# Kernel optimization log

Hardware: AMD Instinct MI355X
Metric: run time of the kernel (lower is better)

## Reference

```python
import jax, jax.numpy as jnp
import numpy as np

N_NODES = 50000
N_EDGES = 1600000
IN_FEATS = 128
HIDDEN = 128
NUM_CLASSES = 40


def setup_inputs() -> dict:
    key = jax.random.key(0)
    k1, k2, k3, k4, k5 = jax.random.split(key, 5)
    features = jax.random.normal(k1, (N_NODES, IN_FEATS), dtype=jnp.float32)
    src = jax.random.randint(k2, (N_EDGES,), 0, N_NODES, dtype=jnp.int32)
    dst = jax.random.randint(k3, (N_EDGES,), 0, N_NODES, dtype=jnp.int32)
    W1 = jax.random.normal(k4, (IN_FEATS, HIDDEN), dtype=jnp.float32) / np.sqrt(IN_FEATS)
    b1 = jnp.zeros((HIDDEN,), dtype=jnp.float32)
    W2 = jax.random.normal(k5, (HIDDEN, NUM_CLASSES), dtype=jnp.float32) / np.sqrt(HIDDEN)
    b2 = jnp.zeros((NUM_CLASSES,), dtype=jnp.float32)
    return {"features": features, "src": src, "dst": dst,
            "W1": W1, "b1": b1, "W2": W2, "b2": b2}


def _degree_norms(src, dst, n_nodes):
    ones = jnp.ones(src.shape[0], dtype=jnp.float32)
    deg_out = jax.ops.segment_sum(ones, src, num_segments=n_nodes)
    deg_in = jax.ops.segment_sum(ones, dst, num_segments=n_nodes)
    # DGL GraphConv clamps degree at 1 (zero-degree nodes get norm 1)
    norm_src = jax.lax.rsqrt(jnp.maximum(deg_out, 1.0))
    norm_dst = jax.lax.rsqrt(jnp.maximum(deg_in, 1.0))
    return norm_src, norm_dst


def _graph_conv(x, W, b, src, dst, norm_src, norm_dst, n_nodes):
    # norm='both': h = D_in^{-1/2} A^T (D_out^{-1/2} x W) + b
    h = (x * norm_src[:, None]) @ W          # [N, out]
    msgs = h[src]                             # gather  [E, out]
    agg = jax.ops.segment_sum(msgs, dst, num_segments=n_nodes)  # scatter-add [N, out]
    return agg * norm_dst[:, None] + b


def reference(features, src, dst, W1, b1, W2, b2):
    n = features.shape[0]
    norm_src, norm_dst = _degree_norms(src, dst, n)
    h = jax.nn.relu(_graph_conv(features, W1, b1, src, dst, norm_src, norm_dst, n))
    h = _graph_conv(h, W2, b2, src, dst, norm_src, norm_dst, n)
    return h
```

## Files before the change

### kernel.cpp

```cpp
#include <hip/hip_runtime.h>


#define CHUNK 16384
#define CHUNK_SHIFT 14
#define NSLICES 64

typedef int iv4 __attribute__((ext_vector_type(4)));
typedef short short8 __attribute__((ext_vector_type(8)));
typedef float f32x4 __attribute__((ext_vector_type(4)));

__device__ __forceinline__ unsigned f2bf_bits(float f) {
    unsigned u = __float_as_uint(f);
    return (u + 0x7FFFu + ((u >> 16) & 1u)) >> 16;
}
__device__ __forceinline__ unsigned pack_bf2(float a, float b) {
    return f2bf_bits(a) | (f2bf_bits(b) << 16);
}
__device__ __forceinline__ float bflo(unsigned v) { return __uint_as_float(v << 16); }
__device__ __forceinline__ float bfhi(unsigned v) { return __uint_as_float(v & 0xFFFF0000u); }


__global__ __launch_bounds__(256) void count_kernel(const int* __restrict__ src, const int* __restrict__ dst,
                                                    unsigned int* __restrict__ part, int E, int per) {
    __shared__ unsigned int h[CHUNK];
    int c = blockIdx.y, s = blockIdx.x, t = threadIdx.x;
    #pragma unroll
    for (int i = 0; i < CHUNK / 256; ++i) h[i * 256 + t] = 0;
    __syncthreads();
    int base = c << CHUNK_SHIFT;
    int beg = s * per;
    int end = min(E, beg + per);
    int nv = (end - beg) >> 2;
    const iv4* d4 = (const iv4*)(dst + beg);
    const iv4* s4 = (const iv4*)(src + beg);
    for (int i = t; i < nv; i += 256) {
        iv4 dv = __builtin_nontemporal_load(d4 + i);
        iv4 sv = __builtin_nontemporal_load(s4 + i);
        int x;
        x = dv.x - base; if ((unsigned)x < CHUNK) atomicAdd(&h[x], 1u);
        x = dv.y - base; if ((unsigned)x < CHUNK) atomicAdd(&h[x], 1u);
        x = dv.z - base; if ((unsigned)x < CHUNK) atomicAdd(&h[x], 1u);
        x = dv.w - base; if ((unsigned)x < CHUNK) atomicAdd(&h[x], 1u);
        x = sv.x - base; if ((unsigned)x < CHUNK) atomicAdd(&h[x], 0x10000u);
        x = sv.y - base; if ((unsigned)x < CHUNK) atomicAdd(&h[x], 0x10000u);
        x = sv.z - base; if ((unsigned)x < CHUNK) atomicAdd(&h[x], 0x10000u);
        x = sv.w - base; if ((unsigned)x < CHUNK) atomicAdd(&h[x], 0x10000u);
    }
    for (int e = beg + (nv << 2) + t; e < end; e += 256) {
        int x = dst[e] - base; if ((unsigned)x < CHUNK) atomicAdd(&h[x], 1u);
        x = src[e] - base;     if ((unsigned)x < CHUNK) atomicAdd(&h[x], 0x10000u);
    }
    __syncthreads();
    unsigned int* out = part + (((size_t)(c * NSLICES + s)) << CHUNK_SHIFT);
    #pragma unroll
    for (int i = 0; i < CHUNK / 256; ++i) __builtin_nontemporal_store(h[i * 256 + t], out + i * 256 + t);
}

__global__ __launch_bounds__(256) void reduce_kernel(const unsigned int* __restrict__ part,
                                                     float* __restrict__ norm_src, float* __restrict__ norm_dst,
                                                     int* __restrict__ deg_dst_i, int N) {
    int d = blockIdx.x * 256 + threadIdx.x;
    if (d >= N) return;
    int c = d >> CHUNK_SHIFT, idx = d & (CHUNK - 1);
    const unsigned int* p = part + (((size_t)c * NSLICES) << CHUNK_SHIFT) + idx;
    unsigned int dsum = 0, ssum = 0;
    #pragma unroll
    for (int s = 0; s < NSLICES; ++s) {
        unsigned int v = __builtin_nontemporal_load(p + ((size_t)s << CHUNK_SHIFT));
        dsum += v & 0xFFFFu;
        ssum += v >> 16;
    }
    deg_dst_i[d] = (int)dsum;
    norm_src[d] = rsqrtf(fmaxf((float)ssum, 1.0f));
    norm_dst[d] = rsqrtf(fmaxf((float)dsum, 1.0f));
}

__global__ __launch_bounds__(256) void scanA_kernel(const int* __restrict__ deg, int* __restrict__ bsum, int N) {
    __shared__ int wsum[4];
    int b = blockIdx.x, t = threadIdx.x, lane = t & 63, wid = t >> 6;
    int i0 = b * 1024 + t * 4;
    int s = 0;
    if (i0 + 3 < N) {
        int4 v = *(const int4*)(deg + i0);
        s = v.x + v.y + v.z + v.w;
    } else {
        for (int k = 0; k < 4; ++k) { int i = i0 + k; if (i < N) s += deg[i]; }
    }
    #pragma unroll
    for (int off = 32; off; off >>= 1) s += __shfl_down(s, off, 64);
    if (lane == 0) wsum[wid] = s;
    __syncthreads();
    if (t == 0) bsum[b] = wsum[0] + wsum[1] + wsum[2] + wsum[3];
}

__global__ __launch_bounds__(64) void scanB_kernel(int* __restrict__ bsum, int NB,
                                                   int* __restrict__ row_ptr, int N) {
    int t = threadIdx.x;
    int v = (t < NB) ? bsum[t] : 0;
    int x = v;
    #pragma unroll
    for (int off = 1; off < 64; off <<= 1) {
        int y = __shfl_up(x, off, 64);
        if (t >= off) x += y;
    }
    if (t < NB) bsum[t] = x - v;
    if (t == 63) row_ptr[N] = x;
}

__global__ __launch_bounds__(256) void scanC_kernel(const int* __restrict__ deg, const int* __restrict__ bsum,
                                                    int* __restrict__ row_ptr, int N) {
    __shared__ int wsum[4];
    int b = blockIdx.x, t = threadIdx.x, lane = t & 63, wid = t >> 6;
    int i0 = b * 1024 + t * 4;
    int4 v = make_int4(0, 0, 0, 0);
    if (i0 + 3 < N) v = *(const int4*)(deg + i0);
    else {
        v.x = (i0 < N) ? deg[i0] : 0;
        v.y = (i0 + 1 < N) ? deg[i0 + 1] : 0;
        v.z = (i0 + 2 < N) ? deg[i0 + 2] : 0;
        v.w = (i0 + 3 < N) ? deg[i0 + 3] : 0;
    }
    int tsum = v.x + v.y + v.z + v.w;
    int x = tsum;
    #pragma unroll
    for (int off = 1; off < 64; off <<= 1) {
        int y = __shfl_up(x, off, 64);
        if (lane >= off) x += y;
    }
    if (lane == 63) wsum[wid] = x;
    __syncthreads();
    int woff = 0;
    for (int k = 0; k < wid; ++k) woff += wsum[k];
    int base = bsum[b] + woff + (x - tsum);
    int e0 = base, e1 = e0 + v.x, e2 = e1 + v.y, e3 = e2 + v.z;
    if (i0 + 3 < N) *(int4*)(row_ptr + i0) = make_int4(e0, e1, e2, e3);
    else {
        if (i0 < N) row_ptr[i0] = e0;
        if (i0 + 1 < N) row_ptr[i0 + 1] = e1;
        if (i0 + 2 < N) row_ptr[i0 + 2] = e2;
        if (i0 + 3 < N) row_ptr[i0 + 3] = e3;
    }
}

__global__ __launch_bounds__(256) void offsets_kernel(unsigned int* __restrict__ part,
                                                      const int* __restrict__ row_ptr, int N) {
    int d = blockIdx.x * 256 + threadIdx.x;
    if (d >= N) return;
    int c = d >> CHUNK_SHIFT, idx = d & (CHUNK - 1);
    unsigned int* p = part + (((size_t)c * NSLICES) << CHUNK_SHIFT) + idx;
    unsigned int running = (unsigned int)row_ptr[d];
    #pragma unroll
    for (int s = 0; s < NSLICES; ++s) {
        unsigned int v = __builtin_nontemporal_load(p + ((size_t)s << CHUNK_SHIFT));
        __builtin_nontemporal_store(running, p + ((size_t)s << CHUNK_SHIFT));
        running += v & 0xFFFFu;
    }
}

__global__ __launch_bounds__(256) void scatter_kernel(const int* __restrict__ src, const int* __restrict__ dst,
                                                      const unsigned int* __restrict__ cum,
                                                      int* __restrict__ col, int E, int per) {
    __shared__ int cur[CHUNK];
    int c = blockIdx.y, s = blockIdx.x, t = threadIdx.x;
    const unsigned int* cc = cum + (((size_t)(c * NSLICES + s)) << CHUNK_SHIFT);
    #pragma unroll
    for (int i = 0; i < CHUNK / 256; ++i) cur[i * 256 + t] = (int)__builtin_nontemporal_load(cc + i * 256 + t);
    __syncthreads();
    int base = c << CHUNK_SHIFT;
    int beg = s * per;
    int end = min(E, beg + per);
    int nv = (end - beg) >> 2;
    const iv4* d4 = (const iv4*)(dst + beg);
    const iv4* s4 = (const iv4*)(src + beg);
    for (int i = t; i < nv; i += 256) {
        iv4 dv = __builtin_nontemporal_load(d4 + i);
        iv4 sv = __builtin_nontemporal_load(s4 + i);
        int x;
        x = dv.x - base; if ((unsigned)x < CHUNK) col[atomicAdd(&cur[x], 1)] = sv.x;
        x = dv.y - base; if ((unsigned)x < CHUNK) col[atomicAdd(&cur[x], 1)] = sv.y;
        x = dv.z - base; if ((unsigned)x < CHUNK) col[atomicAdd(&cur[x], 1)] = sv.z;
        x = dv.w - base; if ((unsigned)x < CHUNK) col[atomicAdd(&cur[x], 1)] = sv.w;
    }
    for (int e = beg + (nv << 2) + t; e < end; e += 256) {
        int x = dst[e] - base;
        if ((unsigned)x < CHUNK) col[atomicAdd(&cur[x], 1)] = src[e];
    }
}


__global__ __launch_bounds__(256) void wprep_kernel(const float* __restrict__ W, unsigned short* __restrict__ wt) {
    int tid = blockIdx.x * 256 + threadIdx.x;
    int c = tid & 127, kg = tid >> 7;
    unsigned p[4];
    #pragma unroll
    for (int j = 0; j < 4; ++j) {
        float v0 = W[(kg * 8 + 2 * j) * 128 + c];
        float v1 = W[(kg * 8 + 2 * j + 1) * 128 + c];
        p[j] = pack_bf2(v0, v1);
    }
    *(uint4*)(wt + (size_t)c * 128 + kg * 8) = make_uint4(p[0], p[1], p[2], p[3]);
}

__global__ __launch_bounds__(256) void gemm1_kernel(const float* __restrict__ x, const float* __restrict__ norm,
                                                    const unsigned short* __restrict__ wt,
                                                    unsigned short* __restrict__ h1u, int N) {
    __shared__ uint4 xs4[1024];
    char* xsb = (char*)xs4;
    int t = threadIdx.x;
    int rb = blockIdx.x * 64;
    #pragma unroll
    for (int i = 0; i < 8; ++i) {
        int idx = i * 256 + t;
        int row = idx >> 5, k4 = (idx & 31) << 2;
        int gr = rb + row;
        float4 v = make_float4(0.f, 0.f, 0.f, 0.f);
        if (gr < N) {
            v = *(const float4*)(x + (size_t)gr * 128 + k4);
            float nm = norm[gr];
            v.x *= nm; v.y *= nm; v.z *= nm; v.w *= nm;
        }
        int boff = row * 256 + ((k4 * 2) ^ ((row & 7) << 4));
        *(uint2*)(xsb + boff) = make_uint2(pack_bf2(v.x, v.y), pack_bf2(v.z, v.w));
    }
    __syncthreads();
    int w = t >> 6, lane = t & 63;
    int lrow = lane & 15, g = lane >> 4;
    int sw = (lrow & 7) << 4;
    int rloc = (w << 4) + lrow;
    short8 a[4];
    #pragma unroll
    for (int kt = 0; kt < 4; ++kt)
        a[kt] = *(const short8*)(xsb + rloc * 256 + ((kt * 64 + g * 16) ^ sw));
    f32x4 acc[8];
    #pragma unroll
    for (int ct = 0; ct < 8; ++ct) acc[ct] = (f32x4){0.f, 0.f, 0.f, 0.f};
    #pragma unroll
    for (int ct = 0; ct < 8; ++ct) {
        const unsigned short* wb = wt + (size_t)(ct * 16 + lrow) * 128 + g * 8;
        short8 b0 = *(const short8*)(wb);
        short8 b1 = *(const short8*)(wb + 32);
        short8 b2 = *(const short8*)(wb + 64);
        short8 b3 = *(const short8*)(wb + 96);
        acc[ct] = __builtin_amdgcn_mfma_f32_16x16x32_bf16(a[0], b0, acc[ct], 0, 0, 0);
        acc[ct] = __builtin_amdgcn_mfma_f32_16x16x32_bf16(a[1], b1, acc[ct], 0, 0, 0);
        acc[ct] = __builtin_amdgcn_mfma_f32_16x16x32_bf16(a[2], b2, acc[ct], 0, 0, 0);
        acc[ct] = __builtin_amdgcn_mfma_f32_16x16x32_bf16(a[3], b3, acc[ct], 0, 0, 0);
    }
    int rbase = rb + (w << 4) + g * 4;
    #pragma unroll
    for (int reg = 0; reg < 4; ++reg) {
        int rowg = rbase + reg;
        if (rowg < N) {
            #pragma unroll
            for (int ct = 0; ct < 8; ++ct)
                h1u[(size_t)rowg * 128 + ct * 16 + lrow] = (unsigned short)f2bf_bits(acc[ct][reg]);
        }
    }
}


#define ACC8(v)  { a0 += bflo(v.x); a1 += bfhi(v.x); a2 += bflo(v.y); a3 += bfhi(v.y); \
                   a4 += bflo(v.z); a5 += bfhi(v.z); a6 += bflo(v.w); a7 += bfhi(v.w); }

__global__ __launch_bounds__(256) void agg1_kernel(const int* __restrict__ row_ptr, const int* __restrict__ col,
                                                   const uint4* __restrict__ h1q, const float* __restrict__ norm_dst,
                                                   const float* __restrict__ norm_src,
                                                   const float* __restrict__ b1, uint4* __restrict__ yq, int N) {
    int t = threadIdx.x;
    int wid = t >> 6, lane = t & 63;
    int g = lane >> 4, f = lane & 15;
    int n = blockIdx.x * 4 + wid;
    if (n >= N) return;
    int beg = row_ptr[n], deg = row_ptr[n + 1] - beg;
    const int* cp = col + beg;
    float a0 = 0, a1 = 0, a2 = 0, a3 = 0, a4 = 0, a5 = 0, a6 = 0, a7 = 0;
    int e = 0;
    for (; e + 8 <= deg; e += 8) {
        int s0 = cp[e + g];
        int s1 = cp[e + 4 + g];
        uint4 v0 = h1q[(size_t)s0 * 16 + f];
        uint4 v1 = h1q[(size_t)s1 * 16 + f];
        ACC8(v0); ACC8(v1);
    }
    for (; e < deg; e += 4) {
        int idx = e + g;
        if (idx < deg) {
            uint4 v = h1q[(size_t)cp[idx] * 16 + f];
            ACC8(v);
        }
    }
    a0 += __shfl_xor(a0, 16, 64); a0 += __shfl_xor(a0, 32, 64);
    a1 += __shfl_xor(a1, 16, 64); a1 += __shfl_xor(a1, 32, 64);
    a2 += __shfl_xor(a2, 16, 64); a2 += __shfl_xor(a2, 32, 64);
    a3 += __shfl_xor(a3, 16, 64); a3 += __shfl_xor(a3, 32, 64);
    a4 += __shfl_xor(a4, 16, 64); a4 += __shfl_xor(a4, 32, 64);
    a5 += __shfl_xor(a5, 16, 64); a5 += __shfl_xor(a5, 32, 64);
    a6 += __shfl_xor(a6, 16, 64); a6 += __shfl_xor(a6, 32, 64);
    a7 += __shfl_xor(a7, 16, 64); a7 += __shfl_xor(a7, 32, 64);
    if (g == 0) {
        float nd = norm_dst[n];
        float ns = norm_src[n];
        float4 bA = *(const float4*)(b1 + f * 8);
        float4 bB = *(const float4*)(b1 + f * 8 + 4);
        float o0 = ns * fmaxf(a0 * nd + bA.x, 0.f);
        float o1 = ns * fmaxf(a1 * nd + bA.y, 0.f);
        float o2 = ns * fmaxf(a2 * nd + bA.z, 0.f);
        float o3 = ns * fmaxf(a3 * nd + bA.w, 0.f);
        float o4 = ns * fmaxf(a4 * nd + bB.x, 0.f);
        float o5 = ns * fmaxf(a5 * nd + bB.y, 0.f);
        float o6 = ns * fmaxf(a6 * nd + bB.z, 0.f);
        float o7 = ns * fmaxf(a7 * nd + bB.w, 0.f);
        uint4 p;
        p.x = pack_bf2(o0, o1); p.y = pack_bf2(o2, o3);
        p.z = pack_bf2(o4, o5); p.w = pack_bf2(o6, o7);
        yq[(size_t)n * 16 + f] = p;
    }
}

__global__ __launch_bounds__(256) void aggY_kernel(const int* __restrict__ row_ptr, const int* __restrict__ col,
                                                   const uint4* __restrict__ yq, const float* __restrict__ norm_dst,
                                                   uint4* __restrict__ zq, int N) {
    int t = threadIdx.x;
    int wid = t >> 6, lane = t & 63;
    int g = lane >> 4, f = lane & 15;
    int n = blockIdx.x * 4 + wid;
    if (n >= N) return;
    int beg = row_ptr[n], deg = row_ptr[n + 1] - beg;
    const int* cp = col + beg;
    float a0 = 0, a1 = 0, a2 = 0, a3 = 0, a4 = 0, a5 = 0, a6 = 0, a7 = 0;
    int e = 0;
    for (; e + 8 <= deg; e += 8) {
        int s0 = cp[e + g];
        int s1 = cp[e + 4 + g];
        uint4 v0 = yq[(size_t)s0 * 16 + f];
        uint4 v1 = yq[(size_t)s1 * 16 + f];
        ACC8(v0); ACC8(v1);
    }
    for (; e < deg; e += 4) {
        int idx = e + g;
        if (idx < deg) {
            uint4 v = yq[(size_t)cp[idx] * 16 + f];
            ACC8(v);
        }
    }
    a0 += __shfl_xor(a0, 16, 64); a0 += __shfl_xor(a0, 32, 64);
    a1 += __shfl_xor(a1, 16, 64); a1 += __shfl_xor(a1, 32, 64);
    a2 += __shfl_xor(a2, 16, 64); a2 += __shfl_xor(a2, 32, 64);
    a3 += __shfl_xor(a3, 16, 64); a3 += __shfl_xor(a3, 32, 64);
    a4 += __shfl_xor(a4, 16, 64); a4 += __shfl_xor(a4, 32, 64);
    a5 += __shfl_xor(a5, 16, 64); a5 += __shfl_xor(a5, 32, 64);
    a6 += __shfl_xor(a6, 16, 64); a6 += __shfl_xor(a6, 32, 64);
    a7 += __shfl_xor(a7, 16, 64); a7 += __shfl_xor(a7, 32, 64);
    if (g == 0) {
        float nd = norm_dst[n];
        uint4 p;
        p.x = pack_bf2(a0 * nd, a1 * nd); p.y = pack_bf2(a2 * nd, a3 * nd);
        p.z = pack_bf2(a4 * nd, a5 * nd); p.w = pack_bf2(a6 * nd, a7 * nd);
        zq[(size_t)n * 16 + f] = p;
    }
}

__global__ __launch_bounds__(256) void gemmOut_kernel(const unsigned int* __restrict__ zp,
                                                      const float* __restrict__ W, const float* __restrict__ b2,
                                                      float* __restrict__ out, int N) {
    __shared__ float xs[128 * 64];
    __shared__ float ws2[128 * 40];
    int t = threadIdx.x;
    int rb = blockIdx.x * 64;
    #pragma unroll
    for (int i = 0; i < 5; ++i) {
        int idx = i * 256 + t;
        *(float4*)(ws2 + idx * 4) = *(const float4*)(W + idx * 4);
    }
    #pragma unroll
    for (int i = 0; i < 16; ++i) {
        int idx = i * 256 + t;
        int row = idx >> 6, kp = idx & 63;
        int gr = rb + row;
        unsigned v = 0;
        if (gr < N) v = zp[(size_t)gr * 64 + kp];
        int r = row ^ (((kp >> 1) & 7) << 2);
        xs[(2 * kp + 0) * 64 + r] = bflo(v);
        xs[(2 * kp + 1) * 64 + r] = bfhi(v);
    }
    __syncthreads();
    int jg = t & 7, rg = t >> 3;
    int j = jg * 5, r0 = rg << 1;
    float acc0[5] = {0, 0, 0, 0, 0};
    float acc1[5] = {0, 0, 0, 0, 0};
    #pragma unroll 4
    for (int k = 0; k < 128; ++k) {
        int sw = ((k >> 2) & 7) << 2;
        float2 xv = *(const float2*)&xs[k * 64 + (r0 ^ sw)];
        #pragma unroll
        for (int c = 0; c < 5; ++c) {
            float w = ws2[k * 40 + j + c];
            acc0[c] += xv.x * w;
            acc1[c] += xv.y * w;
        }
    }
    int gr0 = rb + r0;
    if (gr0 < N) {
        #pragma unroll
        for (int c = 0; c < 5; ++c) out[(size_t)gr0 * 40 + j + c] = acc0[c] + b2[j + c];
    }
    if (gr0 + 1 < N) {
        #pragma unroll
        for (int c = 0; c < 5; ++c) out[(size_t)(gr0 + 1) * 40 + j + c] = acc1[c] + b2[j + c];
    }
}

extern "C" void kernel_launch(void* const* d_in, const int* in_sizes, int n_in,
                              void* d_out, int out_size, void* d_ws, size_t ws_size,
                              hipStream_t stream) {
    const float* x  = (const float*)d_in[0];
    const int* src  = (const int*)d_in[1];
    const int* dst  = (const int*)d_in[2];
    const float* W1 = (const float*)d_in[3];
    const float* b1 = (const float*)d_in[4];
    const float* W2 = (const float*)d_in[5];
    const float* b2 = (const float*)d_in[6];
    float* out = (float*)d_out;

    int N = in_sizes[0] / 128;
    int E = in_sizes[1];
    int NPAD = (N + 63) & ~63;
    int NCHUNKS = (N + CHUNK - 1) >> CHUNK_SHIFT;
    int per = ((E + NSLICES - 1) / NSLICES + 3) & ~3;
    int NB = (N + 1023) / 1024;

    float* ws = (float*)d_ws;
    float* norm_src = ws;
    float* norm_dst = ws + NPAD;
    int* deg_dst_i  = (int*)(ws + 2 * (size_t)NPAD);
    int* row_ptr    = (int*)(ws + 3 * (size_t)NPAD);
    int* bsum       = (int*)(ws + 4 * (size_t)NPAD);
    unsigned short* wt1 = (unsigned short*)(ws + 4 * (size_t)NPAD + 64);
    int* col        = (int*)(ws + 4 * (size_t)NPAD + 64 + 8192);
    size_t h1_off   = ((size_t)4 * NPAD + 64 + 8192 + E + 15) & ~(size_t)15;
    unsigned short* h1u = (unsigned short*)(ws + h1_off);
    uint4* h1q      = (uint4*)h1u;
    uint4* yq       = h1q + (size_t)NPAD * 16;
    uint4* zq       = h1q;
    unsigned int* zp = (unsigned int*)zq;
    unsigned int* part = (unsigned int*)h1u;

    dim3 cgrid(NSLICES, NCHUNKS);
    wprep_kernel<<<8, 256, 0, stream>>>(W1, wt1);
    count_kernel<<<cgrid, 256, 0, stream>>>(src, dst, part, E, per);
    reduce_kernel<<<(N + 255) / 256, 256, 0, stream>>>(part, norm_src, norm_dst, deg_dst_i, N);
    scanA_kernel<<<NB, 256, 0, stream>>>(deg_dst_i, bsum, N);
    scanB_kernel<<<1, 64, 0, stream>>>(bsum, NB, row_ptr, N);
    scanC_kernel<<<NB, 256, 0, stream>>>(deg_dst_i, bsum, row_ptr, N);
    offsets_kernel<<<(N + 255) / 256, 256, 0, stream>>>(part, row_ptr, N);
    scatter_kernel<<<cgrid, 256, 0, stream>>>(src, dst, part, col, E, per);
    gemm1_kernel<<<(N + 63) / 64, 256, 0, stream>>>(x, norm_src, wt1, h1u, N);
    agg1_kernel<<<(N + 3) / 4, 256, 0, stream>>>(row_ptr, col, h1q, norm_dst, norm_src, b1, yq, N);
    aggY_kernel<<<(N + 3) / 4, 256, 0, stream>>>(row_ptr, col, yq, norm_dst, zq, N);
    gemmOut_kernel<<<(N + 63) / 64, 256, 0, stream>>>(zp, W2, b2, out, N);
}
```

Before: 238.2 us.

## Split feature columns into 32-wide tiles and pin each tile to an XCD pair

The hidden features are stored column-tiled, with four tiles of 32 bf16 columns each laid out as separate [NPAD,32] planes. Blocks of the aggregation kernels are remapped so that each pair of XCDs handles one feature tile. This is meant to shrink the working set each XCD's L2 must cache for the random neighbor gathers, from 12.8MB to 3.2MB per tile. Each edge's gather is now a 64-byte row segment read with more edges processed in parallel per wavefront, at the cost of reading the column indices four times and doing a longer shuffle reduction.

```diff
diff --git a/kernel.cpp b/kernel.cpp
--- a/kernel.cpp
+++ b/kernel.cpp
@@ -203,7 +203,7 @@
 
 __global__ __launch_bounds__(256) void gemm1_kernel(const float* __restrict__ x, const float* __restrict__ norm,
                                                     const unsigned short* __restrict__ wt,
-                                                    unsigned short* __restrict__ h1u, int N) {
+                                                    unsigned short* __restrict__ h1u, int N, int NPAD) {
     __shared__ uint4 xs4[1024];
     char* xsb = (char*)xs4;
     int t = threadIdx.x;
@@ -252,8 +252,11 @@
         int rowg = rbase + reg;
         if (rowg < N) {
             #pragma unroll
-            for (int ct = 0; ct < 8; ++ct)
-                h1u[(size_t)rowg * 128 + ct * 16 + lrow] = (unsigned short)f2bf_bits(acc[ct][reg]);
+            for (int ct = 0; ct < 8; ++ct) {
+                int c = ct * 16 + lrow;
+                h1u[(size_t)(c >> 5) * NPAD * 32 + (size_t)rowg * 32 + (c & 31)] =
+                    (unsigned short)f2bf_bits(acc[ct][reg]);
+            }
         }
     }
 }
@@ -261,47 +264,53 @@
 
 #define ACC8(v)  { a0 += bflo(v.x); a1 += bfhi(v.x); a2 += bflo(v.y); a3 += bfhi(v.y); \
                    a4 += bflo(v.z); a5 += bfhi(v.z); a6 += bflo(v.w); a7 += bfhi(v.w); }
+#define RED16()  { a0 += __shfl_xor(a0, 4, 64); a0 += __shfl_xor(a0, 8, 64); a0 += __shfl_xor(a0, 16, 64); a0 += __shfl_xor(a0, 32, 64); \
+                   a1 += __shfl_xor(a1, 4, 64); a1 += __shfl_xor(a1, 8, 64); a1 += __shfl_xor(a1, 16, 64); a1 += __shfl_xor(a1, 32, 64); \
+                   a2 += __shfl_xor(a2, 4, 64); a2 += __shfl_xor(a2, 8, 64); a2 += __shfl_xor(a2, 16, 64); a2 += __shfl_xor(a2, 32, 64); \
+                   a3 += __shfl_xor(a3, 4, 64); a3 += __shfl_xor(a3, 8, 64); a3 += __shfl_xor(a3, 16, 64); a3 += __shfl_xor(a3, 32, 64); \
+                   a4 += __shfl_xor(a4, 4, 64); a4 += __shfl_xor(a4, 8, 64); a4 += __shfl_xor(a4, 16, 64); a4 += __shfl_xor(a4, 32, 64); \
+                   a5 += __shfl_xor(a5, 4, 64); a5 += __shfl_xor(a5, 8, 64); a5 += __shfl_xor(a5, 16, 64); a5 += __shfl_xor(a5, 32, 64); \
+                   a6 += __shfl_xor(a6, 4, 64); a6 += __shfl_xor(a6, 8, 64); a6 += __shfl_xor(a6, 16, 64); a6 += __shfl_xor(a6, 32, 64); \
+                   a7 += __shfl_xor(a7, 4, 64); a7 += __shfl_xor(a7, 8, 64); a7 += __shfl_xor(a7, 16, 64); a7 += __shfl_xor(a7, 32, 64); }
 
 __global__ __launch_bounds__(256) void agg1_kernel(const int* __restrict__ row_ptr, const int* __restrict__ col,
-                                                   const uint4* __restrict__ h1q, const float* __restrict__ norm_dst,
-                                                   const float* __restrict__ norm_src,
-                                                   const float* __restrict__ b1, uint4* __restrict__ yq, int N) {
-    int t = threadIdx.x;
-    int wid = t >> 6, lane = t & 63;
-    int g = lane >> 4, f = lane & 15;
-    int n = blockIdx.x * 4 + wid;
+                                                   const uint4* __restrict__ h1t, const float* __restrict__ norm_dst,
+                                                   const float* __restrict__ norm_src, const float* __restrict__ b1,
+                                                   uint4* __restrict__ yt, int N, int NPAD, int Bt) {
+    int bid = blockIdx.x;
+    int xcd = bid & 7, tile = xcd >> 1;
+    int nblk = (bid >> 3) * 2 + (xcd & 1);
+    if (nblk >= Bt) return;
+    int t = threadIdx.x, wid = t >> 6, lane = t & 63;
+    int g = lane >> 2, f = lane & 3;
+    int n = nblk * 4 + wid;
     if (n >= N) return;
     int beg = row_ptr[n], deg = row_ptr[n + 1] - beg;
     const int* cp = col + beg;
+    const uint4* hb = h1t + (size_t)tile * NPAD * 4 + f;
     float a0 = 0, a1 = 0, a2 = 0, a3 = 0, a4 = 0, a5 = 0, a6 = 0, a7 = 0;
     int e = 0;
-    for (; e + 8 <= deg; e += 8) {
-        int s0 = cp[e + g];
-        int s1 = cp[e + 4 + g];
-        uint4 v0 = h1q[(size_t)s0 * 16 + f];
-        uint4 v1 = h1q[(size_t)s1 * 16 + f];
+    for (; e + 32 <= deg; e += 32) {
+        int s0 = __builtin_nontemporal_load(cp + e + g);
+        int s1 = __builtin_nontemporal_load(cp + e + 16 + g);
+        uint4 v0 = hb[(size_t)s0 * 4];
+        uint4 v1 = hb[(size_t)s1 * 4];
         ACC8(v0); ACC8(v1);
     }
-    for (; e < deg; e += 4) {
+    for (; e < deg; e += 16) {
         int idx = e + g;
         if (idx < deg) {
-            uint4 v = h1q[(size_t)cp[idx] * 16 + f];
+            uint4 v = hb[(size_t)__builtin_nontemporal_load(cp + idx) * 4];
             ACC8(v);
         }
     }
-    a0 += __shfl_xor(a0, 16, 64); a0 += __shfl_xor(a0, 32, 64);
-    a1 += __shfl_xor(a1, 16, 64); a1 += __shfl_xor(a1, 32, 64);
-    a2 += __shfl_xor(a2, 16, 64); a2 += __shfl_xor(a2, 32, 64);
-    a3 += __shfl_xor(a3, 16, 64); a3 += __shfl_xor(a3, 32, 64);
-    a4 += __shfl_xor(a4, 16, 64); a4 += __shfl_xor(a4, 32, 64);
-    a5 += __shfl_xor(a5, 16, 64); a5 += __shfl_xor(a5, 32, 64);
-    a6 += __shfl_xor(a6, 16, 64); a6 += __shfl_xor(a6, 32, 64);
-    a7 += __shfl_xor(a7, 16, 64); a7 += __shfl_xor(a7, 32, 64);
+    RED16();
     if (g == 0) {
         float nd = norm_dst[n];
         float ns = norm_src[n];
-        float4 bA = *(const float4*)(b1 + f * 8);
-        float4 bB = *(const float4*)(b1 + f * 8 + 4);
+        const float* bb = b1 + tile * 32 + f * 8;
+        float4 bA = *(const float4*)(bb);
+        float4 bB = *(const float4*)(bb + 4);
         float o0 = ns * fmaxf(a0 * nd + bA.x, 0.f);
         float o1 = ns * fmaxf(a1 * nd + bA.y, 0.f);
         float o2 = ns * fmaxf(a2 * nd + bA.z, 0.f);
@@ -313,56 +322,53 @@
         uint4 p;
         p.x = pack_bf2(o0, o1); p.y = pack_bf2(o2, o3);
         p.z = pack_bf2(o4, o5); p.w = pack_bf2(o6, o7);
-        yq[(size_t)n * 16 + f] = p;
+        yt[(size_t)tile * NPAD * 4 + (size_t)n * 4 + f] = p;
     }
 }
 
 __global__ __launch_bounds__(256) void aggY_kernel(const int* __restrict__ row_ptr, const int* __restrict__ col,
-                                                   const uint4* __restrict__ yq, const float* __restrict__ norm_dst,
-                                                   uint4* __restrict__ zq, int N) {
-    int t = threadIdx.x;
-    int wid = t >> 6, lane = t & 63;
-    int g = lane >> 4, f = lane & 15;
-    int n = blockIdx.x * 4 + wid;
+                                                   const uint4* __restrict__ yt, const float* __restrict__ norm_dst,
+                                                   uint4* __restrict__ zt, int N, int NPAD, int Bt) {
+    int bid = blockIdx.x;
+    int xcd = bid & 7, tile = xcd >> 1;
+    int nblk = (bid >> 3) * 2 + (xcd & 1);
+    if (nblk >= Bt) return;
+    int t = threadIdx.x, wid = t >> 6, lane = t & 63;
+    int g = lane >> 2, f = lane & 3;
+    int n = nblk * 4 + wid;
     if (n >= N) return;
     int beg = row_ptr[n], deg = row_ptr[n + 1] - beg;
     const int* cp = col + beg;
+    const uint4* hb = yt + (size_t)tile * NPAD * 4 + f;
     float a0 = 0, a1 = 0, a2 = 0, a3 = 0, a4 = 0, a5 = 0, a6 = 0, a7 = 0;
     int e = 0;
-    for (; e + 8 <= deg; e += 8) {
-        int s0 = cp[e + g];
-        int s1 = cp[e + 4 + g];
-        uint4 v0 = yq[(size_t)s0 * 16 + f];
-        uint4 v1 = yq[(size_t)s1 * 16 + f];
+    for (; e + 32 <= deg; e += 32) {
+        int s0 = __builtin_nontemporal_load(cp + e + g);
+        int s1 = __builtin_nontemporal_load(cp + e + 16 + g);
+        uint4 v0 = hb[(size_t)s0 * 4];
+        uint4 v1 = hb[(size_t)s1 * 4];
         ACC8(v0); ACC8(v1);
     }
-    for (; e < deg; e += 4) {
+    for (; e < deg; e += 16) {
         int idx = e + g;
         if (idx < deg) {
-            uint4 v = yq[(size_t)cp[idx] * 16 + f];
+            uint4 v = hb[(size_t)__builtin_nontemporal_load(cp + idx) * 4];
             ACC8(v);
         }
     }
-    a0 += __shfl_xor(a0, 16, 64); a0 += __shfl_xor(a0, 32, 64);
-    a1 += __shfl_xor(a1, 16, 64); a1 += __shfl_xor(a1, 32, 64);
-    a2 += __shfl_xor(a2, 16, 64); a2 += __shfl_xor(a2, 32, 64);
-    a3 += __shfl_xor(a3, 16, 64); a3 += __shfl_xor(a3, 32, 64);
-    a4 += __shfl_xor(a4, 16, 64); a4 += __shfl_xor(a4, 32, 64);
-    a5 += __shfl_xor(a5, 16, 64); a5 += __shfl_xor(a5, 32, 64);
-    a6 += __shfl_xor(a6, 16, 64); a6 += __shfl_xor(a6, 32, 64);
-    a7 += __shfl_xor(a7, 16, 64); a7 += __shfl_xor(a7, 32, 64);
+    RED16();
     if (g == 0) {
         float nd = norm_dst[n];
         uint4 p;
         p.x = pack_bf2(a0 * nd, a1 * nd); p.y = pack_bf2(a2 * nd, a3 * nd);
         p.z = pack_bf2(a4 * nd, a5 * nd); p.w = pack_bf2(a6 * nd, a7 * nd);
-        zq[(size_t)n * 16 + f] = p;
+        zt[(size_t)tile * NPAD * 4 + (size_t)n * 4 + f] = p;
     }
 }
 
 __global__ __launch_bounds__(256) void gemmOut_kernel(const unsigned int* __restrict__ zp,
                                                       const float* __restrict__ W, const float* __restrict__ b2,
-                                                      float* __restrict__ out, int N) {
+                                                      float* __restrict__ out, int N, int NPAD) {
     __shared__ float xs[128 * 64];
     __shared__ float ws2[128 * 40];
     int t = threadIdx.x;
@@ -378,7 +384,7 @@
         int row = idx >> 6, kp = idx & 63;
         int gr = rb + row;
         unsigned v = 0;
-        if (gr < N) v = zp[(size_t)gr * 64 + kp];
+        if (gr < N) v = zp[(size_t)(kp >> 4) * NPAD * 16 + (size_t)gr * 16 + (kp & 15)];
         int r = row ^ (((kp >> 1) & 7) << 2);
         xs[(2 * kp + 0) * 64 + r] = bflo(v);
         xs[(2 * kp + 1) * 64 + r] = bfhi(v);
@@ -454,8 +460,10 @@
     scanC_kernel<<<NB, 256, 0, stream>>>(deg_dst_i, bsum, row_ptr, N);
     offsets_kernel<<<(N + 255) / 256, 256, 0, stream>>>(part, row_ptr, N);
     scatter_kernel<<<cgrid, 256, 0, stream>>>(src, dst, part, col, E, per);
-    gemm1_kernel<<<(N + 63) / 64, 256, 0, stream>>>(x, norm_src, wt1, h1u, N);
-    agg1_kernel<<<(N + 3) / 4, 256, 0, stream>>>(row_ptr, col, h1q, norm_dst, norm_src, b1, yq, N);
-    aggY_kernel<<<(N + 3) / 4, 256, 0, stream>>>(row_ptr, col, yq, norm_dst, zq, N);
-    gemmOut_kernel<<<(N + 63) / 64, 256, 0, stream>>>(zp, W2, b2, out, N);
-}
+    gemm1_kernel<<<(N + 63) / 64, 256, 0, stream>>>(x, norm_src, wt1, h1u, N, NPAD);
+    int Bt = (N + 3) / 4;
+    int P = (Bt + 1) / 2;
+    agg1_kernel<<<8 * P, 256, 0, stream>>>(row_ptr, col, h1q, norm_dst, norm_src, b1, yq, N, NPAD, Bt);
+    aggY_kernel<<<8 * P, 256, 0, stream>>>(row_ptr, col, yq, norm_dst, zq, N, NPAD, Bt);
+    gemmOut_kernel<<<(N + 63) / 64, 256, 0, stream>>>(zp, W2, b2, out, N, NPAD);
+}
```

Result: slower. 327.6 us (+37.5%).

## Apply W2 before second-layer aggregation to shrink gathered rows to 40 classes

Applied to the files above, without the earlier changes.

Reorders the second graph convolution so the 128-to-40 projection happens before neighbor aggregation, using a new MFMA bf16 GEMM kernel with W2 pre-packed into a padded 48-wide bf16 layout. The edge gather then reads 64-element (128-byte) rows instead of 128-element rows, which roughly halves the gather traffic in the second aggregation. The fp32 output GEMM is removed, and bias plus norm_dst are applied directly in the aggregation epilogue. In exchange it adds an extra bf16 rounding of the projected values before summation and wastes some lanes on padded columns.

```diff
diff --git a/kernel.cpp b/kernel.cpp
--- a/kernel.cpp
+++ b/kernel.cpp
@@ -201,6 +201,19 @@
     *(uint4*)(wt + (size_t)c * 128 + kg * 8) = make_uint4(p[0], p[1], p[2], p[3]);
 }
 
+__global__ __launch_bounds__(256) void wprep2_kernel(const float* __restrict__ W2, unsigned short* __restrict__ wt2) {
+    int tid = blockIdx.x * 256 + threadIdx.x;
+    int c = tid >> 4, kg = tid & 15;
+    unsigned p[4];
+    #pragma unroll
+    for (int j = 0; j < 4; ++j) {
+        float v0 = (c < 40) ? W2[(kg * 8 + 2 * j) * 40 + c] : 0.f;
+        float v1 = (c < 40) ? W2[(kg * 8 + 2 * j + 1) * 40 + c] : 0.f;
+        p[j] = pack_bf2(v0, v1);
+    }
+    *(uint4*)(wt2 + (size_t)c * 128 + kg * 8) = make_uint4(p[0], p[1], p[2], p[3]);
+}
+
 __global__ __launch_bounds__(256) void gemm1_kernel(const float* __restrict__ x, const float* __restrict__ norm,
                                                     const unsigned short* __restrict__ wt,
                                                     unsigned short* __restrict__ h1u, int N) {
@@ -254,6 +267,60 @@
             #pragma unroll
             for (int ct = 0; ct < 8; ++ct)
                 h1u[(size_t)rowg * 128 + ct * 16 + lrow] = (unsigned short)f2bf_bits(acc[ct][reg]);
+        }
+    }
+}
+
+__global__ __launch_bounds__(256) void gemmW2_kernel(const unsigned short* __restrict__ yu,
+                                                     const unsigned short* __restrict__ wt2,
+                                                     unsigned short* __restrict__ wu, int N) {
+    __shared__ uint4 xs4[1024];
+    char* xsb = (char*)xs4;
+    int t = threadIdx.x;
+    int rb = blockIdx.x * 64;
+    #pragma unroll
+    for (int i = 0; i < 8; ++i) {
+        int idx = i * 256 + t;
+        int row = idx >> 5, q = idx & 31;
+        int gr = rb + row;
+        uint2 v = make_uint2(0u, 0u);
+        if (gr < N) v = *(const uint2*)(yu + (size_t)gr * 128 + q * 4);
+        int boff = row * 256 + ((q * 8) ^ ((row & 7) << 4));
+        *(uint2*)(xsb + boff) = v;
+    }
+    __syncthreads();
+    int w = t >> 6, lane = t & 63;
+    int lrow = lane & 15, g = lane >> 4;
+    int sw = (lrow & 7) << 4;
+    int rloc = (w << 4) + lrow;
+    short8 a[4];
+    #pragma unroll
+    for (int kt = 0; kt < 4; ++kt)
+        a[kt] = *(const short8*)(xsb + rloc * 256 + ((kt * 64 + g * 16) ^ sw));
+    f32x4 acc[3];
+    #pragma unroll
+    for (int ct = 0; ct < 3; ++ct) acc[ct] = (f32x4){0.f, 0.f, 0.f, 0.f};
+    #pragma unroll
+    for (int ct = 0; ct < 3; ++ct) {
+        const unsigned short* wb = wt2 + (size_t)(ct * 16 + lrow) * 128 + g * 8;
+        short8 b0 = *(const short8*)(wb);
+        short8 b1 = *(const short8*)(wb + 32);
+        short8 b2 = *(const short8*)(wb + 64);
+        short8 b3 = *(const short8*)(wb + 96);
+        acc[ct] = __builtin_amdgcn_mfma_f32_16x16x32_bf16(a[0], b0, acc[ct], 0, 0, 0);
+        acc[ct] = __builtin_amdgcn_mfma_f32_16x16x32_bf16(a[1], b1, acc[ct], 0, 0, 0);
+        acc[ct] = __builtin_amdgcn_mfma_f32_16x16x32_bf16(a[2], b2, acc[ct], 0, 0, 0);
+        acc[ct] = __builtin_amdgcn_mfma_f32_16x16x32_bf16(a[3], b3, acc[ct], 0, 0, 0);
+    }
+    int rbase = rb + (w << 4) + g * 4;
+    #pragma unroll
+    for (int reg = 0; reg < 4; ++reg) {
+        int rowg = rbase + reg;
+        if (rowg < N) {
+            #pragma unroll
+            for (int ct = 0; ct < 3; ++ct)
+                wu[(size_t)rowg * 64 + ct * 16 + lrow] = (unsigned short)f2bf_bits(acc[ct][reg]);
+            wu[(size_t)rowg * 64 + 48 + lrow] = 0;
         }
     }
 }
@@ -317,96 +384,48 @@
     }
 }
 
-__global__ __launch_bounds__(256) void aggY_kernel(const int* __restrict__ row_ptr, const int* __restrict__ col,
-                                                   const uint4* __restrict__ yq, const float* __restrict__ norm_dst,
-                                                   uint4* __restrict__ zq, int N) {
+__global__ __launch_bounds__(256) void aggZ_kernel(const int* __restrict__ row_ptr, const int* __restrict__ col,
+                                                   const uint4* __restrict__ wq, const float* __restrict__ norm_dst,
+                                                   const float* __restrict__ b2, float* __restrict__ out, int N) {
     int t = threadIdx.x;
     int wid = t >> 6, lane = t & 63;
-    int g = lane >> 4, f = lane & 15;
+    int g = lane >> 3, f = lane & 7;
     int n = blockIdx.x * 4 + wid;
     if (n >= N) return;
     int beg = row_ptr[n], deg = row_ptr[n + 1] - beg;
     const int* cp = col + beg;
     float a0 = 0, a1 = 0, a2 = 0, a3 = 0, a4 = 0, a5 = 0, a6 = 0, a7 = 0;
     int e = 0;
-    for (; e + 8 <= deg; e += 8) {
+    for (; e + 16 <= deg; e += 16) {
         int s0 = cp[e + g];
-        int s1 = cp[e + 4 + g];
-        uint4 v0 = yq[(size_t)s0 * 16 + f];
-        uint4 v1 = yq[(size_t)s1 * 16 + f];
+        int s1 = cp[e + 8 + g];
+        uint4 v0 = wq[(size_t)s0 * 8 + f];
+        uint4 v1 = wq[(size_t)s1 * 8 + f];
         ACC8(v0); ACC8(v1);
     }
-    for (; e < deg; e += 4) {
+    for (; e < deg; e += 8) {
         int idx = e + g;
         if (idx < deg) {
-            uint4 v = yq[(size_t)cp[idx] * 16 + f];
+            uint4 v = wq[(size_t)cp[idx] * 8 + f];
             ACC8(v);
         }
     }
-    a0 += __shfl_xor(a0, 16, 64); a0 += __shfl_xor(a0, 32, 64);
-    a1 += __shfl_xor(a1, 16, 64); a1 += __shfl_xor(a1, 32, 64);
-    a2 += __shfl_xor(a2, 16, 64); a2 += __shfl_xor(a2, 32, 64);
-    a3 += __shfl_xor(a3, 16, 64); a3 += __shfl_xor(a3, 32, 64);
-    a4 += __shfl_xor(a4, 16, 64); a4 += __shfl_xor(a4, 32, 64);
-    a5 += __shfl_xor(a5, 16, 64); a5 += __shfl_xor(a5, 32, 64);
-    a6 += __shfl_xor(a6, 16, 64); a6 += __shfl_xor(a6, 32, 64);
-    a7 += __shfl_xor(a7, 16, 64); a7 += __shfl_xor(a7, 32, 64);
-    if (g == 0) {
+    a0 += __shfl_xor(a0, 8, 64); a0 += __shfl_xor(a0, 16, 64); a0 += __shfl_xor(a0, 32, 64);
+    a1 += __shfl_xor(a1, 8, 64); a1 += __shfl_xor(a1, 16, 64); a1 += __shfl_xor(a1, 32, 64);
+    a2 += __shfl_xor(a2, 8, 64); a2 += __shfl_xor(a2, 16, 64); a2 += __shfl_xor(a2, 32, 64);
+    a3 += __shfl_xor(a3, 8, 64); a3 += __shfl_xor(a3, 16, 64); a3 += __shfl_xor(a3, 32, 64);
+    a4 += __shfl_xor(a4, 8, 64); a4 += __shfl_xor(a4, 16, 64); a4 += __shfl_xor(a4, 32, 64);
+    a5 += __shfl_xor(a5, 8, 64); a5 += __shfl_xor(a5, 16, 64); a5 += __shfl_xor(a5, 32, 64);
+    a6 += __shfl_xor(a6, 8, 64); a6 += __shfl_xor(a6, 16, 64); a6 += __shfl_xor(a6, 32, 64);
+    a7 += __shfl_xor(a7, 8, 64); a7 += __shfl_xor(a7, 16, 64); a7 += __shfl_xor(a7, 32, 64);
+    if (g == 0 && f < 5) {
         float nd = norm_dst[n];
-        uint4 p;
-        p.x = pack_bf2(a0 * nd, a1 * nd); p.y = pack_bf2(a2 * nd, a3 * nd);
-        p.z = pack_bf2(a4 * nd, a5 * nd); p.w = pack_bf2(a6 * nd, a7 * nd);
-        zq[(size_t)n * 16 + f] = p;
-    }
-}
-
-__global__ __launch_bounds__(256) void gemmOut_kernel(const unsigned int* __restrict__ zp,
-                                                      const float* __restrict__ W, const float* __restrict__ b2,
-                                                      float* __restrict__ out, int N) {
-    __shared__ float xs[128 * 64];
-    __shared__ float ws2[128 * 40];
-    int t = threadIdx.x;
-    int rb = blockIdx.x * 64;
-    #pragma unroll
-    for (int i = 0; i < 5; ++i) {
-        int idx = i * 256 + t;
-        *(float4*)(ws2 + idx * 4) = *(const float4*)(W + idx * 4);
-    }
-    #pragma unroll
-    for (int i = 0; i < 16; ++i) {
-        int idx = i * 256 + t;
-        int row = idx >> 6, kp = idx & 63;
-        int gr = rb + row;
-        unsigned v = 0;
-        if (gr < N) v = zp[(size_t)gr * 64 + kp];
-        int r = row ^ (((kp >> 1) & 7) << 2);
-        xs[(2 * kp + 0) * 64 + r] = bflo(v);
-        xs[(2 * kp + 1) * 64 + r] = bfhi(v);
-    }
-    __syncthreads();
-    int jg = t & 7, rg = t >> 3;
-    int j = jg * 5, r0 = rg << 1;
-    float acc0[5] = {0, 0, 0, 0, 0};
-    float acc1[5] = {0, 0, 0, 0, 0};
-    #pragma unroll 4
-    for (int k = 0; k < 128; ++k) {
-        int sw = ((k >> 2) & 7) << 2;
-        float2 xv = *(const float2*)&xs[k * 64 + (r0 ^ sw)];
-        #pragma unroll
-        for (int c = 0; c < 5; ++c) {
-            float w = ws2[k * 40 + j + c];
-            acc0[c] += xv.x * w;
-            acc1[c] += xv.y * w;
-        }
-    }
-    int gr0 = rb + r0;
-    if (gr0 < N) {
-        #pragma unroll
-        for (int c = 0; c < 5; ++c) out[(size_t)gr0 * 40 + j + c] = acc0[c] + b2[j + c];
-    }
-    if (gr0 + 1 < N) {
-        #pragma unroll
-        for (int c = 0; c < 5; ++c) out[(size_t)(gr0 + 1) * 40 + j + c] = acc1[c] + b2[j + c];
+        int j0 = f * 8;
+        float4 bA = *(const float4*)(b2 + j0);
+        float4 bB = *(const float4*)(b2 + j0 + 4);
+        float* op = out + (size_t)n * 40 + j0;
+        *(float4*)(op)     = make_float4(a0 * nd + bA.x, a1 * nd + bA.y, a2 * nd + bA.z, a3 * nd + bA.w);
+        *(float4*)(op + 4) = make_float4(a4 * nd + bB.x, a5 * nd + bB.y, a6 * nd + bB.z, a7 * nd + bB.w);
     }
 }
 
@@ -436,17 +455,20 @@
     int* row_ptr    = (int*)(ws + 3 * (size_t)NPAD);
     int* bsum       = (int*)(ws + 4 * (size_t)NPAD);
     unsigned short* wt1 = (unsigned short*)(ws + 4 * (size_t)NPAD + 64);
-    int* col        = (int*)(ws + 4 * (size_t)NPAD + 64 + 8192);
-    size_t h1_off   = ((size_t)4 * NPAD + 64 + 8192 + E + 15) & ~(size_t)15;
+    unsigned short* wt2 = (unsigned short*)(ws + 4 * (size_t)NPAD + 64 + 8192);
+    int* col        = (int*)(ws + 4 * (size_t)NPAD + 64 + 8192 + 3072);
+    size_t h1_off   = ((size_t)4 * NPAD + 64 + 8192 + 3072 + E + 15) & ~(size_t)15;
     unsigned short* h1u = (unsigned short*)(ws + h1_off);
     uint4* h1q      = (uint4*)h1u;
-    uint4* yq       = h1q + (size_t)NPAD * 16;
-    uint4* zq       = h1q;
-    unsigned int* zp = (unsigned int*)zq;
+    unsigned short* yu = h1u + (size_t)NPAD * 128;
+    uint4* yq       = (uint4*)yu;
+    unsigned short* wu = h1u;
+    uint4* wq       = (uint4*)wu;
     unsigned int* part = (unsigned int*)h1u;
 
     dim3 cgrid(NSLICES, NCHUNKS);
     wprep_kernel<<<8, 256, 0, stream>>>(W1, wt1);
+    wprep2_kernel<<<3, 256, 0, stream>>>(W2, wt2);
     count_kernel<<<cgrid, 256, 0, stream>>>(src, dst, part, E, per);
     reduce_kernel<<<(N + 255) / 256, 256, 0, stream>>>(part, norm_src, norm_dst, deg_dst_i, N);
     scanA_kernel<<<NB, 256, 0, stream>>>(deg_dst_i, bsum, N);
@@ -456,6 +478,6 @@
     scatter_kernel<<<cgrid, 256, 0, stream>>>(src, dst, part, col, E, per);
     gemm1_kernel<<<(N + 63) / 64, 256, 0, stream>>>(x, norm_src, wt1, h1u, N);
     agg1_kernel<<<(N + 3) / 4, 256, 0, stream>>>(row_ptr, col, h1q, norm_dst, norm_src, b1, yq, N);
-    aggY_kernel<<<(N + 3) / 4, 256, 0, stream>>>(row_ptr, col, yq, norm_dst, zq, N);
-    gemmOut_kernel<<<(N + 63) / 64, 256, 0, stream>>>(zp, W2, b2, out, N);
-}
+    gemmW2_kernel<<<(N + 63) / 64, 256, 0, stream>>>(yu, wt2, wu, N);
+    aggZ_kernel<<<(N + 3) / 4, 256, 0, stream>>>(row_ptr, col, wq, norm_dst, b2, out, N);
+}
```

Result: faster. 208.2 us (-12.6%).
